# Performance work log

Measured on AMD Instinct MI355X. Metric: run time of the kernel, lower is better.

The kernel has to match this reference:

```python
import jax, jax.numpy as jnp
import numpy as np

D_MODEL = 512
N_HEADS = 8
HEAD_DIM = D_MODEL // N_HEADS  # 64


def setup_inputs() -> dict:
    key = jax.random.key(0)
    ks = jax.random.split(key, 12)
    B, SQ, SK = 4, 2048, 2048
    s = 1.0 / np.sqrt(D_MODEL)
    return {
        "query": jax.random.normal(ks[0], (B, SQ, D_MODEL), jnp.float32),
        "key": jax.random.normal(ks[1], (B, SK, D_MODEL), jnp.float32),
        "value": jax.random.normal(ks[2], (B, SK, D_MODEL), jnp.float32),
        "Wq": jax.random.normal(ks[3], (D_MODEL, D_MODEL), jnp.float32) * s,
        "bq": jnp.zeros((D_MODEL,), jnp.float32),
        "Wk": jax.random.normal(ks[4], (D_MODEL, D_MODEL), jnp.float32) * s,
        "bk": jnp.zeros((D_MODEL,), jnp.float32),
        "Wv": jax.random.normal(ks[5], (D_MODEL, D_MODEL), jnp.float32) * s,
        "bv": jnp.zeros((D_MODEL,), jnp.float32),
        "Wo": jax.random.normal(ks[6], (D_MODEL, D_MODEL), jnp.float32) * s,
        "bo": jnp.zeros((D_MODEL,), jnp.float32),
    }


def reference(query, key, value, Wq, bq, Wk, bk, Wv, bv, Wo, bo):
    B, SQ, _ = query.shape
    SK = key.shape[1]
    # QKV projections
    Q = query @ Wq.T + bq  # [B,SQ,D]
    K = key @ Wk.T + bk    # [B,SK,D]
    V = value @ Wv.T + bv  # [B,SK,D]
    # split heads -> [B,H,S,hd]
    Q = Q.reshape(B, SQ, N_HEADS, HEAD_DIM).transpose(0, 2, 1, 3)
    K = K.reshape(B, SK, N_HEADS, HEAD_DIM).transpose(0, 2, 1, 3)
    V = V.reshape(B, SK, N_HEADS, HEAD_DIM).transpose(0, 2, 1, 3)
    scale = jnp.sqrt(jnp.float32(HEAD_DIM))
    scores = jnp.einsum('bhqd,bhkd->bhqk', Q, K) / scale  # [B,H,SQ,SK]
    attn = jax.nn.softmax(scores, axis=-1)  # dropout p=0 (eval)
    ctx = jnp.einsum('bhqk,bhkd->bhqd', attn, V)
    ctx = ctx.transpose(0, 2, 1, 3).reshape(B, SQ, D_MODEL)
    # exact (erf) GELU as in torch F.gelu default
    out = jax.nn.gelu(ctx, approximate=False) @ Wo.T + bo
    return out
```

## Files before the change

kernel.cpp:

```cpp
#include <hip/hip_runtime.h>
#include <hip/hip_bf16.h>

#define D_MODEL 512
#define N_HEADS 8
#define HEAD_DIM 64
#define BATCH 4
#define SEQ 2048

typedef _Float16 f16;
typedef _Float16 f16x8 __attribute__((ext_vector_type(8)));
typedef _Float16 f16x4 __attribute__((ext_vector_type(4)));
typedef float f32x4 __attribute__((ext_vector_type(4)));
typedef unsigned int u32x4 __attribute__((ext_vector_type(4)));

#define MFMA16(a, b, c) __builtin_amdgcn_mfma_f32_16x16x32_f16((a), (b), (c), 0, 0, 0)

#define GLOAD_LDS16(src, dst)                                                   \
    __builtin_amdgcn_global_load_lds(                                           \
        (const __attribute__((address_space(1))) void*)(src),                   \
        (__attribute__((address_space(3))) void*)(dst), 16, 0, 0)

#if __has_builtin(__builtin_amdgcn_exp2f)
#define EXP2(x) __builtin_amdgcn_exp2f(x)
#else
#define EXP2(x) __expf((x) * 0.6931471805599453f)
#endif

#define QSCALE 0.18033688011112042f
#define OFF2 8.656170245333781f

__global__ __launch_bounds__(256) void wsplit(
    const float* __restrict__ w0, const float* __restrict__ w1,
    const float* __restrict__ w2, const float* __restrict__ w3,
    f16* __restrict__ h0, f16* __restrict__ h1,
    f16* __restrict__ h2, f16* __restrict__ h3)
{
    const int j = blockIdx.y;
    const float* s = (j == 0) ? w0 : (j == 1) ? w1 : (j == 2) ? w2 : w3;
    f16* dh = (j == 0) ? h0 : (j == 1) ? h1 : (j == 2) ? h2 : h3;
    const int n4 = (D_MODEL * D_MODEL) >> 2;
    for (int i = blockIdx.x * 256 + threadIdx.x; i < n4; i += gridDim.x * 256) {
        float4 x = ((const float4*)s)[i];
        f16x4 hv = {(f16)x.x, (f16)x.y, (f16)x.z, (f16)x.w};
        ((f16x4*)dh)[i] = hv;
    }
}

__global__ __launch_bounds__(256, 3) void proj_mfma(
    const float* __restrict__ Xq, const float* __restrict__ Xk,
    const float* __restrict__ Xv,
    const f16* __restrict__ Wqh, const f16* __restrict__ Wkh,
    const f16* __restrict__ Wvh,
    const float* __restrict__ bq, const float* __restrict__ bk,
    const float* __restrict__ bv,
    f16* __restrict__ Qh, f16* __restrict__ Kh, f16* __restrict__ Vt)
{
    __shared__ f16 ldsA[128 * 64];
    __shared__ f16 ldsW[128 * 64];

    const int z = blockIdx.z;
    const float* X = (z == 0) ? Xq : (z == 1) ? Xk : Xv;
    const f16* Wh = (z == 0) ? Wqh : (z == 1) ? Wkh : Wvh;
    const float* bias = (z == 0) ? bq : (z == 1) ? bk : bv;

    const int m0 = blockIdx.x * 128;
    const int n0 = blockIdx.y * 128;

    const int tid = threadIdx.x;
    const int w = tid >> 6, l = tid & 63;
    const int lp = l >> 4, lq = l & 15;
    const int wm = w >> 1, wn = w & 1;

    f32x4 acc[4][4] = {};

    for (int kt = 0; kt < D_MODEL; kt += 64) {
        __syncthreads();
        float4 av[4][2];
        int arow[4], aslot[4];
#pragma unroll
        for (int j = 0; j < 4; ++j) {
            const int chunk = j * 256 + tid;
            arow[j] = chunk >> 3;
            aslot[j] = chunk & 7;
            const float* sp = X + (size_t)(m0 + arow[j]) * D_MODEL + kt + aslot[j] * 8;
            av[j][0] = *(const float4*)sp;
            av[j][1] = *(const float4*)(sp + 4);
        }
#pragma unroll
        for (int j = 0; j < 4; ++j) {
            const int cb = j * 256 + w * 64;
            const int chunk = cb + l;
            const int row = chunk >> 3;
            const int slot = (chunk & 7) ^ (row & 7);
            GLOAD_LDS16(Wh + (size_t)(n0 + row) * D_MODEL + kt + slot * 8,
                        ldsW + cb * 8);
        }
#pragma unroll
        for (int j = 0; j < 4; ++j) {
            f16x8 hv;
            hv[0] = (f16)av[j][0].x; hv[1] = (f16)av[j][0].y;
            hv[2] = (f16)av[j][0].z; hv[3] = (f16)av[j][0].w;
            hv[4] = (f16)av[j][1].x; hv[5] = (f16)av[j][1].y;
            hv[6] = (f16)av[j][1].z; hv[7] = (f16)av[j][1].w;
            *(f16x8*)(ldsA + arow[j] * 64 + ((aslot[j] ^ (arow[j] & 7)) << 3)) = hv;
        }
        __syncthreads();

        f16x8 af[4][2];
#pragma unroll
        for (int mt = 0; mt < 4; ++mt) {
            const int R = wm * 64 + mt * 16 + lq;
#pragma unroll
            for (int s = 0; s < 2; ++s)
                af[mt][s] = *(const f16x8*)(ldsA + R * 64 + (((s * 4 + lp) ^ (R & 7)) << 3));
        }
        __builtin_amdgcn_s_setprio(1);
#pragma unroll
        for (int nt = 0; nt < 4; ++nt) {
            const int R = wn * 64 + nt * 16 + lq;
            f16x8 b0 = *(const f16x8*)(ldsW + R * 64 + (((0 + lp) ^ (R & 7)) << 3));
            f16x8 b1 = *(const f16x8*)(ldsW + R * 64 + (((4 + lp) ^ (R & 7)) << 3));
#pragma unroll
            for (int mt = 0; mt < 4; ++mt) {
                acc[mt][nt] = MFMA16(af[mt][0], b0, acc[mt][nt]);
                acc[mt][nt] = MFMA16(af[mt][1], b1, acc[mt][nt]);
            }
        }
        __builtin_amdgcn_s_setprio(0);
    }

    const int m_base = m0 + wm * 64;
    const int n_base = n0 + wn * 64;
    const int b = m0 / SEQ;
    const int h = n_base >> 6;
    const size_t bh_ = (size_t)b * N_HEADS + h;

    if (z == 0) {
#pragma unroll
        for (int nt = 0; nt < 4; ++nt) {
            const int n = n_base + nt * 16 + lq;
            const float bn = bias[n];
            const int d = n & 63;
#pragma unroll
            for (int mt = 0; mt < 4; ++mt) {
#pragma unroll
                for (int r = 0; r < 4; ++r) {
                    const int s = (m_base + mt * 16 + lp * 4 + r) & (SEQ - 1);
                    Qh[(bh_ * SEQ + s) * 64 + d] = (f16)((acc[mt][nt][r] + bn) * QSCALE);
                }
            }
        }
    } else if (z == 1) {
#pragma unroll
        for (int nt = 0; nt < 4; ++nt) {
            const int n = n_base + nt * 16 + lq;
            const float bn = bias[n];
            const int d = n & 63;
#pragma unroll
            for (int mt = 0; mt < 4; ++mt) {
#pragma unroll
                for (int r = 0; r < 4; ++r) {
                    const int s = (m_base + mt * 16 + lp * 4 + r) & (SEQ - 1);
                    Kh[(bh_ * SEQ + s) * 64 + d] = (f16)(acc[mt][nt][r] + bn);
                }
            }
        }
    } else {
#pragma unroll
        for (int nt = 0; nt < 4; ++nt) {
            const int n = n_base + nt * 16 + lq;
            const float bn = bias[n];
            const int d = n & 63;
#pragma unroll
            for (int mt = 0; mt < 4; ++mt) {
                const int s0 = (m_base + mt * 16 + lp * 4) & (SEQ - 1);
                f16x4 col;
#pragma unroll
                for (int r = 0; r < 4; ++r)
                    col[r] = (f16)(acc[mt][nt][r] + bn);
                *(f16x4*)(Vt + (bh_ * 64 + d) * SEQ + s0) = col;
            }
        }
    }
}

__global__ __launch_bounds__(256, 4) void out_mfma(
    const f16* __restrict__ Gh, const f16* __restrict__ Woh,
    const float* __restrict__ bo, float* __restrict__ Out)
{
    __shared__ f16 ldsA[64 * 64];
    __shared__ f16 ldsW[128 * 64];

    const int m0 = blockIdx.x * 64;
    const int n0 = blockIdx.y * 128;

    const int tid = threadIdx.x;
    const int w = tid >> 6, l = tid & 63;
    const int lp = l >> 4, lq = l & 15;
    const int wm = w >> 1, wn = w & 1;

    f32x4 acc[2][4] = {};

    for (int kt = 0; kt < D_MODEL; kt += 64) {
        __syncthreads();
#pragma unroll
        for (int j = 0; j < 2; ++j) {
            const int cb = j * 256 + w * 64;
            const int chunk = cb + l;
            const int row = chunk >> 3;
            const int slot = (chunk & 7) ^ (row & 7);
            GLOAD_LDS16(Gh + (size_t)(m0 + row) * D_MODEL + kt + slot * 8,
                        ldsA + cb * 8);
        }
#pragma unroll
        for (int j = 0; j < 4; ++j) {
            const int cb = j * 256 + w * 64;
            const int chunk = cb + l;
            const int row = chunk >> 3;
            const int slot = (chunk & 7) ^ (row & 7);
            GLOAD_LDS16(Woh + (size_t)(n0 + row) * D_MODEL + kt + slot * 8,
                        ldsW + cb * 8);
        }
        __syncthreads();

        f16x8 af[2][2];
#pragma unroll
        for (int mt = 0; mt < 2; ++mt) {
            const int R = wm * 32 + mt * 16 + lq;
#pragma unroll
            for (int s = 0; s < 2; ++s)
                af[mt][s] = *(const f16x8*)(ldsA + R * 64 + (((s * 4 + lp) ^ (R & 7)) << 3));
        }
        __builtin_amdgcn_s_setprio(1);
#pragma unroll
        for (int nt = 0; nt < 4; ++nt) {
            const int R = wn * 64 + nt * 16 + lq;
            f16x8 b0 = *(const f16x8*)(ldsW + R * 64 + (((0 + lp) ^ (R & 7)) << 3));
            f16x8 b1 = *(const f16x8*)(ldsW + R * 64 + (((4 + lp) ^ (R & 7)) << 3));
#pragma unroll
            for (int mt = 0; mt < 2; ++mt) {
                acc[mt][nt] = MFMA16(af[mt][0], b0, acc[mt][nt]);
                acc[mt][nt] = MFMA16(af[mt][1], b1, acc[mt][nt]);
            }
        }
        __builtin_amdgcn_s_setprio(0);
    }

#pragma unroll
    for (int nt = 0; nt < 4; ++nt) {
        const int n = n0 + wn * 64 + nt * 16 + lq;
        const float bn = bo[n];
#pragma unroll
        for (int mt = 0; mt < 2; ++mt) {
#pragma unroll
            for (int r = 0; r < 4; ++r) {
                const int m = m0 + wm * 32 + mt * 16 + lp * 4 + r;
                Out[(size_t)m * D_MODEL + n] = acc[mt][nt][r] + bn;
            }
        }
    }
}

__global__ __launch_bounds__(256, 2) void flash_mfma(
    const f16* __restrict__ Qh, const f16* __restrict__ Kh,
    const f16* __restrict__ Vt, f16* __restrict__ Gh)
{
    __shared__ f16 KV[4][2][4096];

    const int tid = threadIdx.x;
    const int w  = tid >> 6;
    const int l  = tid & 63;
    const int lp = l >> 4;
    const int lq = l & 15;

    const int id = blockIdx.x;
    const int work = (id & 7) * 64 + (id >> 3);
    const int bh = work >> 4;
    const int b  = bh >> 3, h = bh & 7;
    const int q0 = (work & 15) * 128 + w * 32;

    f16x8 qf[2][2];
#pragma unroll
    for (int sub = 0; sub < 2; ++sub)
#pragma unroll
        for (int s = 0; s < 2; ++s)
            qf[sub][s] = *(const f16x8*)(Qh + ((size_t)bh * SEQ + q0 + sub * 16 + lq) * 64
                                          + s * 32 + lp * 8);

    f16x8 ones;
#pragma unroll
    for (int i = 0; i < 8; ++i) ones[i] = (f16)1.f;
    const f32x4 OFFI = (f32x4){-OFF2, -OFF2, -OFF2, -OFF2};

    f32x4 o[2][4];
#pragma unroll
    for (int sub = 0; sub < 2; ++sub)
#pragma unroll
        for (int c = 0; c < 4; ++c) o[sub][c] = (f32x4){0.f, 0.f, 0.f, 0.f};
    f32x4 lf[2] = {(f32x4){0.f, 0.f, 0.f, 0.f}, (f32x4){0.f, 0.f, 0.f, 0.f}};

    int koff[4][2], voff[2][4];
#pragma unroll
    for (int mt = 0; mt < 4; ++mt) {
        const int krow = mt * 16 + lq;
#pragma unroll
        for (int s = 0; s < 2; ++s)
            koff[mt][s] = krow * 128 + (((4 * s + lp) ^ (krow & 7)) << 4);
    }
#pragma unroll
    for (int s = 0; s < 2; ++s)
#pragma unroll
        for (int nt = 0; nt < 4; ++nt) {
            const int d = nt * 16 + lq;
            voff[s][nt] = d * 128 + (((4 * s + lp) ^ (d & 7)) << 4);
        }

    const int lr0 = w * 8 + (l >> 3);
    const int lr1 = (w + 4) * 8 + (l >> 3);
    const f16* kp0 = Kh + ((size_t)bh * SEQ + lr0) * 64 + (((l & 7) ^ (lr0 & 7)) << 3);
    const f16* kp1 = Kh + ((size_t)bh * SEQ + lr1) * 64 + (((l & 7) ^ (lr1 & 7)) << 3);
    const f16* vp0 = Vt + ((size_t)bh * 64 + lr0) * SEQ + (((l & 7) ^ (lr0 & 7)) << 3);
    const f16* vp1 = Vt + ((size_t)bh * 64 + lr1) * SEQ + (((l & 7) ^ (lr1 & 7)) << 3);

    auto STAGE_PAIR = [&](int pr) {
        f16* KA = &KV[pr * 2][0][0];
        f16* VA = &KV[pr * 2][1][0];
        f16* KB = &KV[pr * 2 + 1][0][0];
        f16* VB = &KV[pr * 2 + 1][1][0];
        GLOAD_LDS16(kp0, KA + w * 512);
        GLOAD_LDS16(kp1, KA + (w + 4) * 512);
        GLOAD_LDS16(vp0, VA + w * 512);
        GLOAD_LDS16(vp1, VA + (w + 4) * 512);
        GLOAD_LDS16(kp0 + 4096, KB + w * 512);
        GLOAD_LDS16(kp1 + 4096, KB + (w + 4) * 512);
        GLOAD_LDS16(vp0 + 64, VB + w * 512);
        GLOAD_LDS16(vp1 + 64, VB + (w + 4) * 512);
        kp0 += 8192; kp1 += 8192;
        vp0 += 128;  vp1 += 128;
    };

    auto QKT = [&](int bf, f32x4 (&st)[2][4], f16x8 (&vbr)[2][4]) {
        const char* Kt_ = (const char*)&KV[bf][0][0];
        const char* Vt_ = (const char*)&KV[bf][1][0];
        __builtin_amdgcn_s_setprio(1);
#pragma unroll
        for (int mt = 0; mt < 4; ++mt) {
            f16x8 ah0 = *(const f16x8*)(Kt_ + koff[mt][0]);
            f16x8 ah1 = *(const f16x8*)(Kt_ + koff[mt][1]);
#pragma unroll
            for (int sub = 0; sub < 2; ++sub) {
                st[sub][mt] = MFMA16(ah0, qf[sub][0], OFFI);
                st[sub][mt] = MFMA16(ah1, qf[sub][1], st[sub][mt]);
            }
        }
        __builtin_amdgcn_s_setprio(0);
#pragma unroll
        for (int s = 0; s < 2; ++s)
#pragma unroll
            for (int nt = 0; nt < 4; ++nt)
                vbr[s][nt] = *(const f16x8*)(Vt_ + voff[s][nt]);
    };

    auto SMPV = [&](f32x4 (&st)[2][4], f16x8 (&vbr)[2][4]) {
        f16x8 pa[2][2];
#pragma unroll
        for (int sub = 0; sub < 2; ++sub) {
            unsigned int pk0[4], pk1[4];
#pragma unroll
            for (int mt = 0; mt < 4; ++mt) {
                float e0 = EXP2(st[sub][mt][0]);
                float e1 = EXP2(st[sub][mt][1]);
                float e2 = EXP2(st[sub][mt][2]);
                float e3 = EXP2(st[sub][mt][3]);
                pk0[mt] = __builtin_bit_cast(unsigned int,
                              __builtin_amdgcn_cvt_pkrtz(e0, e1));
                pk1[mt] = __builtin_bit_cast(unsigned int,
                              __builtin_amdgcn_cvt_pkrtz(e2, e3));
            }
#pragma unroll
            for (int s = 0; s < 2; ++s) {
                unsigned int x0 = pk0[2 * s], y0 = pk0[2 * s + 1];
                unsigned int x1 = pk1[2 * s], y1 = pk1[2 * s + 1];
                asm("v_permlane32_swap_b32 %0, %1" : "+v"(x0), "+v"(y0));
                asm("v_permlane16_swap_b32 %0, %1" : "+v"(x0), "+v"(y0));
                asm("v_permlane32_swap_b32 %0, %1" : "+v"(x1), "+v"(y1));
                asm("v_permlane16_swap_b32 %0, %1" : "+v"(x1), "+v"(y1));
                u32x4 t4 = {x0, x1, y0, y1};
                pa[sub][s] = __builtin_bit_cast(f16x8, t4);
            }
        }
        __builtin_amdgcn_s_setprio(1);
#pragma unroll
        for (int s = 0; s < 2; ++s) {
#pragma unroll
            for (int sub = 0; sub < 2; ++sub) {
                lf[sub] = MFMA16(pa[sub][s], ones, lf[sub]);
#pragma unroll
                for (int nt = 0; nt < 4; ++nt)
                    o[sub][nt] = MFMA16(pa[sub][s], vbr[s][nt], o[sub][nt]);
            }
        }
        __builtin_amdgcn_s_setprio(0);
    };

    f32x4 stE[2][4], stO[2][4];
    f16x8 vbrE[2][4], vbrO[2][4];

    STAGE_PAIR(0);
    int pr = 0;

#pragma unroll 1
    for (int t = 0; t < 16; ++t) {
        asm volatile("s_waitcnt vmcnt(0)" ::: "memory");
        __builtin_amdgcn_s_barrier();
        if (t < 15) STAGE_PAIR(pr ^ 1);
        __builtin_amdgcn_sched_barrier(0);

        QKT(pr * 2, stE, vbrE);
        QKT(pr * 2 + 1, stO, vbrO);
        SMPV(stE, vbrE);
        SMPV(stO, vbrO);

        pr ^= 1;
    }

#pragma unroll
    for (int sub = 0; sub < 2; ++sub) {
#pragma unroll
        for (int j = 0; j < 4; ++j) {
            const float inv = 1.f / lf[sub][j];
            const int row = q0 + sub * 16 + lp * 4 + j;
#pragma unroll
            for (int nt = 0; nt < 4; ++nt) {
                float x = o[sub][nt][j] * inv;
                float g = 0.5f * x * (1.f + erff(x * 0.70710678118654752f));
                Gh[((size_t)(b * SEQ + row)) * D_MODEL + h * 64 + nt * 16 + lq] = (f16)g;
            }
        }
    }
}

extern "C" void kernel_launch(void* const* d_in, const int* in_sizes, int n_in,
                              void* d_out, int out_size, void* d_ws, size_t ws_size,
                              hipStream_t stream)
{
    const float* query = (const float*)d_in[0];
    const float* key   = (const float*)d_in[1];
    const float* value = (const float*)d_in[2];
    const float* Wq = (const float*)d_in[3];
    const float* bq = (const float*)d_in[4];
    const float* Wk = (const float*)d_in[5];
    const float* bk = (const float*)d_in[6];
    const float* Wv = (const float*)d_in[7];
    const float* bv = (const float*)d_in[8];
    const float* Wo = (const float*)d_in[9];
    const float* bo = (const float*)d_in[10];

    char* ws = (char*)d_ws;
    const size_t MB = 1024 * 1024;
    const size_t KB = 1024;
    f16* Qh = (f16*)(ws + 0 * MB);
    f16* Kh = (f16*)(ws + 8 * MB);
    f16* Vt = (f16*)(ws + 16 * MB);
    f16* Gh = (f16*)(ws + 24 * MB);
    f16* Wqh = (f16*)(ws + 32 * MB);
    f16* Wkh = (f16*)(ws + 32 * MB + 512 * KB);
    f16* Wvh = (f16*)(ws + 33 * MB);
    f16* Woh = (f16*)(ws + 33 * MB + 512 * KB);

    wsplit<<<dim3(64, 4), 256, 0, stream>>>(Wq, Wk, Wv, Wo, Wqh, Wkh, Wvh, Woh);

    proj_mfma<<<dim3(BATCH * SEQ / 128, D_MODEL / 128, 3), 256, 0, stream>>>(
        query, key, value, Wqh, Wkh, Wvh, bq, bk, bv, Qh, Kh, Vt);

    flash_mfma<<<dim3(512), 256, 0, stream>>>(Qh, Kh, Vt, Gh);

    out_mfma<<<dim3(BATCH * SEQ / 64, D_MODEL / 128), 256, 0, stream>>>(
        Gh, Woh, bo, (float*)d_out);
}
```

Measured before the change: 84.58 us.

## Load V fragments straight from global into registers, stage only K in LDS

The flash attention kernel no longer stages V tiles through shared memory. Each lane now loads its V^T fragments directly from global memory into registers at the top of each iteration, and only K is prefetched into LDS with global_load_lds. Explicit vmcnt waits are placed so the V loads can overlap the QK^T MFMAs. This halves LDS use and removes the V LDS reads, at the cost of less coalesced direct global reads. It also drops the guard on the last K prefetch, so the final iteration reads past the current head's K data.

```diff
diff --git a/kernel.cpp b/kernel.cpp
--- a/kernel.cpp
+++ b/kernel.cpp
@@ -265,7 +265,7 @@
     const f16* __restrict__ Qh, const f16* __restrict__ Kh,
     const f16* __restrict__ Vt, f16* __restrict__ Gh)
 {
-    __shared__ f16 KV[4][2][4096];
+    __shared__ f16 Kl[4][4096];
 
     const int tid = threadIdx.x;
     const int w  = tid >> 6;
@@ -299,7 +299,7 @@
         for (int c = 0; c < 4; ++c) o[sub][c] = (f32x4){0.f, 0.f, 0.f, 0.f};
     f32x4 lf[2] = {(f32x4){0.f, 0.f, 0.f, 0.f}, (f32x4){0.f, 0.f, 0.f, 0.f}};
 
-    int koff[4][2], voff[2][4];
+    int koff[4][2];
 #pragma unroll
     for (int mt = 0; mt < 4; ++mt) {
         const int krow = mt * 16 + lq;
@@ -307,46 +307,34 @@
         for (int s = 0; s < 2; ++s)
             koff[mt][s] = krow * 128 + (((4 * s + lp) ^ (krow & 7)) << 4);
     }
-#pragma unroll
-    for (int s = 0; s < 2; ++s)
-#pragma unroll
-        for (int nt = 0; nt < 4; ++nt) {
-            const int d = nt * 16 + lq;
-            voff[s][nt] = d * 128 + (((4 * s + lp) ^ (d & 7)) << 4);
-        }
 
     const int lr0 = w * 8 + (l >> 3);
     const int lr1 = (w + 4) * 8 + (l >> 3);
     const f16* kp0 = Kh + ((size_t)bh * SEQ + lr0) * 64 + (((l & 7) ^ (lr0 & 7)) << 3);
     const f16* kp1 = Kh + ((size_t)bh * SEQ + lr1) * 64 + (((l & 7) ^ (lr1 & 7)) << 3);
-    const f16* vp0 = Vt + ((size_t)bh * 64 + lr0) * SEQ + (((l & 7) ^ (lr0 & 7)) << 3);
-    const f16* vp1 = Vt + ((size_t)bh * 64 + lr1) * SEQ + (((l & 7) ^ (lr1 & 7)) << 3);
-
-    auto STAGE_PAIR = [&](int pr) {
-        f16* KA = &KV[pr * 2][0][0];
-        f16* VA = &KV[pr * 2][1][0];
-        f16* KB = &KV[pr * 2 + 1][0][0];
-        f16* VB = &KV[pr * 2 + 1][1][0];
-        GLOAD_LDS16(kp0, KA + w * 512);
-        GLOAD_LDS16(kp1, KA + (w + 4) * 512);
-        GLOAD_LDS16(vp0, VA + w * 512);
-        GLOAD_LDS16(vp1, VA + (w + 4) * 512);
-        GLOAD_LDS16(kp0 + 4096, KB + w * 512);
-        GLOAD_LDS16(kp1 + 4096, KB + (w + 4) * 512);
-        GLOAD_LDS16(vp0 + 64, VB + w * 512);
-        GLOAD_LDS16(vp1 + 64, VB + (w + 4) * 512);
+
+    const f16* vg[2][4];
+#pragma unroll
+    for (int s = 0; s < 2; ++s)
+#pragma unroll
+        for (int nt = 0; nt < 4; ++nt)
+            vg[s][nt] = Vt + ((size_t)bh * 64 + nt * 16 + lq) * SEQ + s * 32 + lp * 8;
+
+    auto STAGE_K = [&](int pr) {
+        GLOAD_LDS16(kp0, &Kl[pr * 2][w * 512]);
+        GLOAD_LDS16(kp1, &Kl[pr * 2][(w + 4) * 512]);
+        GLOAD_LDS16(kp0 + 4096, &Kl[pr * 2 + 1][w * 512]);
+        GLOAD_LDS16(kp1 + 4096, &Kl[pr * 2 + 1][(w + 4) * 512]);
         kp0 += 8192; kp1 += 8192;
-        vp0 += 128;  vp1 += 128;
     };
 
-    auto QKT = [&](int bf, f32x4 (&st)[2][4], f16x8 (&vbr)[2][4]) {
-        const char* Kt_ = (const char*)&KV[bf][0][0];
-        const char* Vt_ = (const char*)&KV[bf][1][0];
+    auto QKT = [&](const f16* Kt_, f32x4 (&st)[2][4]) {
+        const char* Kc = (const char*)Kt_;
         __builtin_amdgcn_s_setprio(1);
 #pragma unroll
         for (int mt = 0; mt < 4; ++mt) {
-            f16x8 ah0 = *(const f16x8*)(Kt_ + koff[mt][0]);
-            f16x8 ah1 = *(const f16x8*)(Kt_ + koff[mt][1]);
+            f16x8 ah0 = *(const f16x8*)(Kc + koff[mt][0]);
+            f16x8 ah1 = *(const f16x8*)(Kc + koff[mt][1]);
 #pragma unroll
             for (int sub = 0; sub < 2; ++sub) {
                 st[sub][mt] = MFMA16(ah0, qf[sub][0], OFFI);
@@ -354,11 +342,6 @@
             }
         }
         __builtin_amdgcn_s_setprio(0);
-#pragma unroll
-        for (int s = 0; s < 2; ++s)
-#pragma unroll
-            for (int nt = 0; nt < 4; ++nt)
-                vbr[s][nt] = *(const f16x8*)(Vt_ + voff[s][nt]);
     };
 
     auto SMPV = [&](f32x4 (&st)[2][4], f16x8 (&vbr)[2][4]) {
@@ -406,19 +389,30 @@
     f32x4 stE[2][4], stO[2][4];
     f16x8 vbrE[2][4], vbrO[2][4];
 
-    STAGE_PAIR(0);
+    STAGE_K(0);
     int pr = 0;
 
 #pragma unroll 1
     for (int t = 0; t < 16; ++t) {
-        asm volatile("s_waitcnt vmcnt(0)" ::: "memory");
+#pragma unroll
+        for (int s = 0; s < 2; ++s)
+#pragma unroll
+            for (int nt = 0; nt < 4; ++nt) {
+                vbrE[s][nt] = *(const f16x8*)(vg[s][nt]);
+                vbrO[s][nt] = *(const f16x8*)(vg[s][nt] + 64);
+                vg[s][nt] += 128;
+            }
+        asm volatile("s_waitcnt vmcnt(16)" ::: "memory");
         __builtin_amdgcn_s_barrier();
-        if (t < 15) STAGE_PAIR(pr ^ 1);
+        STAGE_K(pr ^ 1);
         __builtin_amdgcn_sched_barrier(0);
 
-        QKT(pr * 2, stE, vbrE);
-        QKT(pr * 2 + 1, stO, vbrO);
+        QKT(&Kl[pr * 2][0], stE);
+        QKT(&Kl[pr * 2 + 1][0], stO);
+
+        asm volatile("s_waitcnt vmcnt(12)" ::: "memory");
         SMPV(stE, vbrE);
+        asm volatile("s_waitcnt vmcnt(4)" ::: "memory");
         SMPV(stO, vbrO);
 
         pr ^= 1;
```

Result: slower. 109.7 us (+29.7%).

## Split attention KV range in two and merge partials in a combine kernel

Applied to the files above, without the earlier changes.

The flash kernel now processes half of the key sequence per block, doubling the grid to 1024 blocks. LDS staging shrinks to one tile per buffer and the launch bound is raised to allow 4 blocks per CU. The aim is more resident waves per CU and better latency hiding. Unnormalized partial outputs go to workspace in f16 and row sums in f32. A new combine kernel adds the two halves, normalizes, and applies the exact GELU. In exchange it adds extra global traffic, an extra launch, and fp16 rounding of unnormalized partial outputs.

```diff
diff --git a/kernel.cpp b/kernel.cpp
--- a/kernel.cpp
+++ b/kernel.cpp
@@ -261,11 +261,11 @@
     }
 }
 
-__global__ __launch_bounds__(256, 2) void flash_mfma(
+__global__ __launch_bounds__(256, 4) void flash_part(
     const f16* __restrict__ Qh, const f16* __restrict__ Kh,
-    const f16* __restrict__ Vt, f16* __restrict__ Gh)
+    const f16* __restrict__ Vt, f16* __restrict__ Op, float* __restrict__ Lp)
 {
-    __shared__ f16 KV[4][2][4096];
+    __shared__ f16 KV[2][2][4096];
 
     const int tid = threadIdx.x;
     const int w  = tid >> 6;
@@ -274,10 +274,12 @@
     const int lq = l & 15;
 
     const int id = blockIdx.x;
-    const int work = (id & 7) * 64 + (id >> 3);
-    const int bh = work >> 4;
-    const int b  = bh >> 3, h = bh & 7;
-    const int q0 = (work & 15) * 128 + w * 32;
+    const int work = (id & 7) * 128 + (id >> 3);
+    const int bh = work >> 5;
+    const int rest = work & 31;
+    const int qblk = rest >> 1;
+    const int split = rest & 1;
+    const int q0 = qblk * 128 + w * 32;
 
     f16x8 qf[2][2];
 #pragma unroll
@@ -317,26 +319,19 @@
 
     const int lr0 = w * 8 + (l >> 3);
     const int lr1 = (w + 4) * 8 + (l >> 3);
-    const f16* kp0 = Kh + ((size_t)bh * SEQ + lr0) * 64 + (((l & 7) ^ (lr0 & 7)) << 3);
-    const f16* kp1 = Kh + ((size_t)bh * SEQ + lr1) * 64 + (((l & 7) ^ (lr1 & 7)) << 3);
-    const f16* vp0 = Vt + ((size_t)bh * 64 + lr0) * SEQ + (((l & 7) ^ (lr0 & 7)) << 3);
-    const f16* vp1 = Vt + ((size_t)bh * 64 + lr1) * SEQ + (((l & 7) ^ (lr1 & 7)) << 3);
-
-    auto STAGE_PAIR = [&](int pr) {
-        f16* KA = &KV[pr * 2][0][0];
-        f16* VA = &KV[pr * 2][1][0];
-        f16* KB = &KV[pr * 2 + 1][0][0];
-        f16* VB = &KV[pr * 2 + 1][1][0];
-        GLOAD_LDS16(kp0, KA + w * 512);
-        GLOAD_LDS16(kp1, KA + (w + 4) * 512);
-        GLOAD_LDS16(vp0, VA + w * 512);
-        GLOAD_LDS16(vp1, VA + (w + 4) * 512);
-        GLOAD_LDS16(kp0 + 4096, KB + w * 512);
-        GLOAD_LDS16(kp1 + 4096, KB + (w + 4) * 512);
-        GLOAD_LDS16(vp0 + 64, VB + w * 512);
-        GLOAD_LDS16(vp1 + 64, VB + (w + 4) * 512);
-        kp0 += 8192; kp1 += 8192;
-        vp0 += 128;  vp1 += 128;
+    const int krow0 = split * 1024;
+    const f16* kp0 = Kh + ((size_t)bh * SEQ + krow0 + lr0) * 64 + (((l & 7) ^ (lr0 & 7)) << 3);
+    const f16* kp1 = Kh + ((size_t)bh * SEQ + krow0 + lr1) * 64 + (((l & 7) ^ (lr1 & 7)) << 3);
+    const f16* vp0 = Vt + ((size_t)bh * 64 + lr0) * SEQ + krow0 + (((l & 7) ^ (lr0 & 7)) << 3);
+    const f16* vp1 = Vt + ((size_t)bh * 64 + lr1) * SEQ + krow0 + (((l & 7) ^ (lr1 & 7)) << 3);
+
+    auto STAGE = [&](int bf) {
+        GLOAD_LDS16(kp0, &KV[bf][0][w * 512]);
+        GLOAD_LDS16(kp1, &KV[bf][0][(w + 4) * 512]);
+        GLOAD_LDS16(vp0, &KV[bf][1][w * 512]);
+        GLOAD_LDS16(vp1, &KV[bf][1][(w + 4) * 512]);
+        kp0 += 4096; kp1 += 4096;
+        vp0 += 64;   vp1 += 64;
     };
 
     auto QKT = [&](int bf, f32x4 (&st)[2][4], f16x8 (&vbr)[2][4]) {
@@ -403,41 +398,62 @@
         __builtin_amdgcn_s_setprio(0);
     };
 
-    f32x4 stE[2][4], stO[2][4];
-    f16x8 vbrE[2][4], vbrO[2][4];
-
-    STAGE_PAIR(0);
-    int pr = 0;
+    f32x4 st[2][4];
+    f16x8 vbr[2][4];
+
+    STAGE(0);
+    int buf = 0;
 
 #pragma unroll 1
     for (int t = 0; t < 16; ++t) {
         asm volatile("s_waitcnt vmcnt(0)" ::: "memory");
         __builtin_amdgcn_s_barrier();
-        if (t < 15) STAGE_PAIR(pr ^ 1);
+        if (t < 15) STAGE(buf ^ 1);
         __builtin_amdgcn_sched_barrier(0);
 
-        QKT(pr * 2, stE, vbrE);
-        QKT(pr * 2 + 1, stO, vbrO);
-        SMPV(stE, vbrE);
-        SMPV(stO, vbrO);
-
-        pr ^= 1;
-    }
-
+        QKT(buf, st, vbr);
+        SMPV(st, vbr);
+        buf ^= 1;
+    }
+
+    f16* op = Op + ((size_t)split * 32 + bh) * SEQ * 64;
+    float* lpp = Lp + ((size_t)split * 32 + bh) * SEQ;
 #pragma unroll
     for (int sub = 0; sub < 2; ++sub) {
 #pragma unroll
         for (int j = 0; j < 4; ++j) {
-            const float inv = 1.f / lf[sub][j];
             const int row = q0 + sub * 16 + lp * 4 + j;
 #pragma unroll
-            for (int nt = 0; nt < 4; ++nt) {
-                float x = o[sub][nt][j] * inv;
-                float g = 0.5f * x * (1.f + erff(x * 0.70710678118654752f));
-                Gh[((size_t)(b * SEQ + row)) * D_MODEL + h * 64 + nt * 16 + lq] = (f16)g;
-            }
-        }
-    }
+            for (int nt = 0; nt < 4; ++nt)
+                op[(size_t)row * 64 + nt * 16 + lq] = (f16)o[sub][nt][j];
+            if (lq == 0) lpp[row] = lf[sub][j];
+        }
+    }
+}
+
+__global__ __launch_bounds__(256) void combine(
+    const f16* __restrict__ Op, const float* __restrict__ Lp,
+    f16* __restrict__ Gh)
+{
+    const int i = blockIdx.x * 256 + threadIdx.x;
+    const int dg = i & 7;
+    const int rowg = i >> 3;
+    const int bh = rowg >> 11;
+    const int row = rowg & (SEQ - 1);
+    const int b = bh >> 3, h = bh & 7;
+
+    const size_t half = (size_t)32 * SEQ * 8;
+    f16x8 a = ((const f16x8*)Op)[(size_t)rowg * 8 + dg];
+    f16x8 c = ((const f16x8*)Op)[half + (size_t)rowg * 8 + dg];
+    const float inv = 1.f / (Lp[rowg] + Lp[32 * SEQ + rowg]);
+
+    f16x8 g;
+#pragma unroll
+    for (int k = 0; k < 8; ++k) {
+        float x = ((float)a[k] + (float)c[k]) * inv;
+        g[k] = (f16)(0.5f * x * (1.f + erff(x * 0.70710678118654752f)));
+    }
+    ((f16x8*)(Gh + ((size_t)(b * SEQ + row)) * D_MODEL + h * 64))[dg] = g;
 }
 
 extern "C" void kernel_launch(void* const* d_in, const int* in_sizes, int n_in,
@@ -467,13 +483,17 @@
     f16* Wkh = (f16*)(ws + 32 * MB + 512 * KB);
     f16* Wvh = (f16*)(ws + 33 * MB);
     f16* Woh = (f16*)(ws + 33 * MB + 512 * KB);
+    f16* Op  = (f16*)(ws + 34 * MB);
+    float* Lp = (float*)(ws + 50 * MB);
 
     wsplit<<<dim3(64, 4), 256, 0, stream>>>(Wq, Wk, Wv, Wo, Wqh, Wkh, Wvh, Woh);
 
     proj_mfma<<<dim3(BATCH * SEQ / 128, D_MODEL / 128, 3), 256, 0, stream>>>(
         query, key, value, Wqh, Wkh, Wvh, bq, bk, bv, Qh, Kh, Vt);
 
-    flash_mfma<<<dim3(512), 256, 0, stream>>>(Qh, Kh, Vt, Gh);
+    flash_part<<<dim3(1024), 256, 0, stream>>>(Qh, Kh, Vt, Op, Lp);
+
+    combine<<<dim3(2048), 256, 0, stream>>>(Op, Lp, Gh);
 
     out_mfma<<<dim3(BATCH * SEQ / 64, D_MODEL / 128), 256, 0, stream>>>(
         Gh, Woh, bo, (float*)d_out);
```

Result: slower. 95.22 us (+12.6%).

## Switch flash attention inner loop to 32x32x16 MFMA tiles

Applied to the files above, without the earlier changes.

Rewrites the attention kernel's QK^T and PV products to use 32x32x16 f16 MFMA instead of 16x16x32, with new LDS offset layout and register fragment shapes. Row sums are now accumulated in VALU from the exponentials and reduced across lane halves at the end via permlane swap and an LDS scratch, replacing the extra MFMA with a ones vector. Tile processing order changes to QKT/SMPV interleaved per tile, reducing live registers. Risks include different MFMA latency/dependency chains and the LDS reuse at the end without a barrier.

```diff
diff --git a/kernel.cpp b/kernel.cpp
--- a/kernel.cpp
+++ b/kernel.cpp
@@ -11,9 +11,11 @@
 typedef _Float16 f16x8 __attribute__((ext_vector_type(8)));
 typedef _Float16 f16x4 __attribute__((ext_vector_type(4)));
 typedef float f32x4 __attribute__((ext_vector_type(4)));
+typedef float f32x16 __attribute__((ext_vector_type(16)));
 typedef unsigned int u32x4 __attribute__((ext_vector_type(4)));
 
 #define MFMA16(a, b, c) __builtin_amdgcn_mfma_f32_16x16x32_f16((a), (b), (c), 0, 0, 0)
+#define MFMA32(a, b, c) __builtin_amdgcn_mfma_f32_32x32x16_f16((a), (b), (c), 0, 0, 0)
 
 #define GLOAD_LDS16(src, dst)                                                   \
     __builtin_amdgcn_global_load_lds(                                           \
@@ -268,10 +270,10 @@
     __shared__ f16 KV[4][2][4096];
 
     const int tid = threadIdx.x;
-    const int w  = tid >> 6;
-    const int l  = tid & 63;
-    const int lp = l >> 4;
-    const int lq = l & 15;
+    const int w   = tid >> 6;
+    const int l   = tid & 63;
+    const int l31 = l & 31;
+    const int hi  = l >> 5;
 
     const int id = blockIdx.x;
     const int work = (id & 7) * 64 + (id >> 3);
@@ -279,41 +281,28 @@
     const int b  = bh >> 3, h = bh & 7;
     const int q0 = (work & 15) * 128 + w * 32;
 
-    f16x8 qf[2][2];
-#pragma unroll
-    for (int sub = 0; sub < 2; ++sub)
-#pragma unroll
-        for (int s = 0; s < 2; ++s)
-            qf[sub][s] = *(const f16x8*)(Qh + ((size_t)bh * SEQ + q0 + sub * 16 + lq) * 64
-                                          + s * 32 + lp * 8);
-
-    f16x8 ones;
-#pragma unroll
-    for (int i = 0; i < 8; ++i) ones[i] = (f16)1.f;
-    const f32x4 OFFI = (f32x4){-OFF2, -OFF2, -OFF2, -OFF2};
-
-    f32x4 o[2][4];
-#pragma unroll
-    for (int sub = 0; sub < 2; ++sub)
-#pragma unroll
-        for (int c = 0; c < 4; ++c) o[sub][c] = (f32x4){0.f, 0.f, 0.f, 0.f};
-    f32x4 lf[2] = {(f32x4){0.f, 0.f, 0.f, 0.f}, (f32x4){0.f, 0.f, 0.f, 0.f}};
-
-    int koff[4][2], voff[2][4];
-#pragma unroll
-    for (int mt = 0; mt < 4; ++mt) {
-        const int krow = mt * 16 + lq;
-#pragma unroll
-        for (int s = 0; s < 2; ++s)
-            koff[mt][s] = krow * 128 + (((4 * s + lp) ^ (krow & 7)) << 4);
-    }
-#pragma unroll
-    for (int s = 0; s < 2; ++s)
-#pragma unroll
-        for (int nt = 0; nt < 4; ++nt) {
-            const int d = nt * 16 + lq;
-            voff[s][nt] = d * 128 + (((4 * s + lp) ^ (d & 7)) << 4);
-        }
+    f16x8 qf[4];
+#pragma unroll
+    for (int ks = 0; ks < 4; ++ks)
+        qf[ks] = *(const f16x8*)(Qh + ((size_t)bh * SEQ + q0 + l31) * 64 + ks * 16 + hi * 8);
+
+    f32x16 OFFI;
+#pragma unroll
+    for (int i = 0; i < 16; ++i) OFFI[i] = -OFF2;
+
+    f32x16 o[2];
+#pragma unroll
+    for (int nt = 0; nt < 2; ++nt)
+#pragma unroll
+        for (int i = 0; i < 16; ++i) o[nt][i] = 0.f;
+    float lf = 0.f;
+
+    int off[2][4];
+#pragma unroll
+    for (int a = 0; a < 2; ++a)
+#pragma unroll
+        for (int bI = 0; bI < 4; ++bI)
+            off[a][bI] = (32 * a + l31) * 128 + (((2 * bI + hi) ^ (l & 7)) << 4);
 
     const int lr0 = w * 8 + (l >> 3);
     const int lr1 = (w + 4) * 8 + (l >> 3);
@@ -339,72 +328,73 @@
         vp0 += 128;  vp1 += 128;
     };
 
-    auto QKT = [&](int bf, f32x4 (&st)[2][4], f16x8 (&vbr)[2][4]) {
+    auto QKT = [&](int bf, f32x16 (&st)[2], f16x8 (&vbr)[4][2]) {
         const char* Kt_ = (const char*)&KV[bf][0][0];
         const char* Vt_ = (const char*)&KV[bf][1][0];
         __builtin_amdgcn_s_setprio(1);
 #pragma unroll
-        for (int mt = 0; mt < 4; ++mt) {
-            f16x8 ah0 = *(const f16x8*)(Kt_ + koff[mt][0]);
-            f16x8 ah1 = *(const f16x8*)(Kt_ + koff[mt][1]);
-#pragma unroll
-            for (int sub = 0; sub < 2; ++sub) {
-                st[sub][mt] = MFMA16(ah0, qf[sub][0], OFFI);
-                st[sub][mt] = MFMA16(ah1, qf[sub][1], st[sub][mt]);
-            }
+        for (int ot = 0; ot < 2; ++ot) {
+            f16x8 a0 = *(const f16x8*)(Kt_ + off[ot][0]);
+            f16x8 a1 = *(const f16x8*)(Kt_ + off[ot][1]);
+            f16x8 a2 = *(const f16x8*)(Kt_ + off[ot][2]);
+            f16x8 a3 = *(const f16x8*)(Kt_ + off[ot][3]);
+            st[ot] = MFMA32(a0, qf[0], OFFI);
+            st[ot] = MFMA32(a1, qf[1], st[ot]);
+            st[ot] = MFMA32(a2, qf[2], st[ot]);
+            st[ot] = MFMA32(a3, qf[3], st[ot]);
         }
         __builtin_amdgcn_s_setprio(0);
 #pragma unroll
-        for (int s = 0; s < 2; ++s)
-#pragma unroll
-            for (int nt = 0; nt < 4; ++nt)
-                vbr[s][nt] = *(const f16x8*)(Vt_ + voff[s][nt]);
+        for (int kk = 0; kk < 4; ++kk)
+#pragma unroll
+            for (int nt = 0; nt < 2; ++nt)
+                vbr[kk][nt] = *(const f16x8*)(Vt_ + off[nt][kk]);
     };
 
-    auto SMPV = [&](f32x4 (&st)[2][4], f16x8 (&vbr)[2][4]) {
-        f16x8 pa[2][2];
-#pragma unroll
-        for (int sub = 0; sub < 2; ++sub) {
-            unsigned int pk0[4], pk1[4];
-#pragma unroll
-            for (int mt = 0; mt < 4; ++mt) {
-                float e0 = EXP2(st[sub][mt][0]);
-                float e1 = EXP2(st[sub][mt][1]);
-                float e2 = EXP2(st[sub][mt][2]);
-                float e3 = EXP2(st[sub][mt][3]);
-                pk0[mt] = __builtin_bit_cast(unsigned int,
-                              __builtin_amdgcn_cvt_pkrtz(e0, e1));
-                pk1[mt] = __builtin_bit_cast(unsigned int,
-                              __builtin_amdgcn_cvt_pkrtz(e2, e3));
-            }
-#pragma unroll
-            for (int s = 0; s < 2; ++s) {
-                unsigned int x0 = pk0[2 * s], y0 = pk0[2 * s + 1];
-                unsigned int x1 = pk1[2 * s], y1 = pk1[2 * s + 1];
+    auto SMPV = [&](f32x16 (&st)[2], f16x8 (&vbr)[4][2]) {
+        unsigned int pkk[2][8];
+        float lfa = 0.f;
+#pragma unroll
+        for (int ot = 0; ot < 2; ++ot) {
+            float e[16];
+#pragma unroll
+            for (int r = 0; r < 16; ++r) e[r] = EXP2(st[ot][r]);
+            lfa += (((e[0] + e[1]) + (e[2] + e[3])) + ((e[4] + e[5]) + (e[6] + e[7])))
+                 + (((e[8] + e[9]) + (e[10] + e[11])) + ((e[12] + e[13]) + (e[14] + e[15])));
+#pragma unroll
+            for (int g = 0; g < 4; ++g) {
+                pkk[ot][2 * g] = __builtin_bit_cast(unsigned int,
+                    __builtin_amdgcn_cvt_pkrtz(e[4 * g], e[4 * g + 1]));
+                pkk[ot][2 * g + 1] = __builtin_bit_cast(unsigned int,
+                    __builtin_amdgcn_cvt_pkrtz(e[4 * g + 2], e[4 * g + 3]));
+            }
+        }
+        lf += lfa;
+        f16x8 pa[4];
+#pragma unroll
+        for (int ot = 0; ot < 2; ++ot)
+#pragma unroll
+            for (int ksp = 0; ksp < 2; ++ksp) {
+                unsigned int x0 = pkk[ot][4 * ksp + 0];
+                unsigned int x1 = pkk[ot][4 * ksp + 1];
+                unsigned int y0 = pkk[ot][4 * ksp + 2];
+                unsigned int y1 = pkk[ot][4 * ksp + 3];
                 asm("v_permlane32_swap_b32 %0, %1" : "+v"(x0), "+v"(y0));
-                asm("v_permlane16_swap_b32 %0, %1" : "+v"(x0), "+v"(y0));
                 asm("v_permlane32_swap_b32 %0, %1" : "+v"(x1), "+v"(y1));
-                asm("v_permlane16_swap_b32 %0, %1" : "+v"(x1), "+v"(y1));
                 u32x4 t4 = {x0, x1, y0, y1};
-                pa[sub][s] = __builtin_bit_cast(f16x8, t4);
-            }
-        }
+                pa[2 * ot + ksp] = __builtin_bit_cast(f16x8, t4);
+            }
         __builtin_amdgcn_s_setprio(1);
 #pragma unroll
-        for (int s = 0; s < 2; ++s) {
-#pragma unroll
-            for (int sub = 0; sub < 2; ++sub) {
-                lf[sub] = MFMA16(pa[sub][s], ones, lf[sub]);
-#pragma unroll
-                for (int nt = 0; nt < 4; ++nt)
-                    o[sub][nt] = MFMA16(pa[sub][s], vbr[s][nt], o[sub][nt]);
-            }
-        }
+        for (int kk = 0; kk < 4; ++kk)
+#pragma unroll
+            for (int nt = 0; nt < 2; ++nt)
+                o[nt] = MFMA32(pa[kk], vbr[kk][nt], o[nt]);
         __builtin_amdgcn_s_setprio(0);
     };
 
-    f32x4 stE[2][4], stO[2][4];
-    f16x8 vbrE[2][4], vbrO[2][4];
+    f32x16 st[2];
+    f16x8 vbr[4][2];
 
     STAGE_PAIR(0);
     int pr = 0;
@@ -416,28 +406,43 @@
         if (t < 15) STAGE_PAIR(pr ^ 1);
         __builtin_amdgcn_sched_barrier(0);
 
-        QKT(pr * 2, stE, vbrE);
-        QKT(pr * 2 + 1, stO, vbrO);
-        SMPV(stE, vbrE);
-        SMPV(stO, vbrO);
+        QKT(pr * 2, st, vbr);
+        SMPV(st, vbr);
+        QKT(pr * 2 + 1, st, vbr);
+        SMPV(st, vbr);
 
         pr ^= 1;
     }
 
-#pragma unroll
-    for (int sub = 0; sub < 2; ++sub) {
-#pragma unroll
-        for (int j = 0; j < 4; ++j) {
-            const float inv = 1.f / lf[sub][j];
-            const int row = q0 + sub * 16 + lp * 4 + j;
-#pragma unroll
-            for (int nt = 0; nt < 4; ++nt) {
-                float x = o[sub][nt][j] * inv;
-                float g = 0.5f * x * (1.f + erff(x * 0.70710678118654752f));
-                Gh[((size_t)(b * SEQ + row)) * D_MODEL + h * 64 + nt * 16 + lq] = (f16)g;
-            }
-        }
-    }
+    float a_ = lf, b_ = lf;
+    asm("v_permlane32_swap_b32 %0, %1" : "+v"(a_), "+v"(b_));
+    const float tot = lf + ((l < 32) ? b_ : a_);
+
+    float* lfb = (float*)&KV[0][0][0] + w * 32;
+    if (l < 32) lfb[l31] = tot;
+    asm volatile("s_waitcnt lgkmcnt(0)" ::: "memory");
+    __builtin_amdgcn_sched_barrier(0);
+
+    f32x4 iv[4];
+#pragma unroll
+    for (int g = 0; g < 4; ++g) {
+        f32x4 tv = *(const f32x4*)(lfb + 8 * g + 4 * hi);
+        iv[g][0] = 1.f / tv[0]; iv[g][1] = 1.f / tv[1];
+        iv[g][2] = 1.f / tv[2]; iv[g][3] = 1.f / tv[3];
+    }
+
+#pragma unroll
+    for (int nt = 0; nt < 2; ++nt)
+#pragma unroll
+        for (int g = 0; g < 4; ++g)
+#pragma unroll
+            for (int r = 0; r < 4; ++r) {
+                const int reg = 4 * g + r;
+                const int row = q0 + 8 * g + 4 * hi + r;
+                float x = o[nt][reg] * iv[g][r];
+                float gl = 0.5f * x * (1.f + erff(x * 0.70710678118654752f));
+                Gh[((size_t)(b * SEQ + row)) * D_MODEL + h * 64 + nt * 32 + l31] = (f16)gl;
+            }
 }
 
 extern "C" void kernel_launch(void* const* d_in, const int* in_sizes, int n_in,
```

Result: slower. 88.77 us (+5.0%).
